# Performance work log

Hardware: AMD Instinct MI355X
Metric: run time of the kernel (lower is better)

Reference implementation:

```python
import jax, jax.numpy as jnp
import numpy as np

C = 512
NUM_HEADS = 8
HEAD_DIM = C // NUM_HEADS


def setup_inputs() -> dict:
    key = jax.random.key(0)
    ks = jax.random.split(key, 9)
    s = 1.0 / np.sqrt(C)
    x = jax.random.normal(ks[0], (8, C, 32, 32), dtype=jnp.float32)
    Wq = jax.random.uniform(ks[1], (C, C), jnp.float32, -s, s)
    bq = jax.random.uniform(ks[2], (C,), jnp.float32, -s, s)
    Wk = jax.random.uniform(ks[3], (C, C), jnp.float32, -s, s)
    bk = jax.random.uniform(ks[4], (C,), jnp.float32, -s, s)
    Wv = jax.random.uniform(ks[5], (C, C), jnp.float32, -s, s)
    bv = jax.random.uniform(ks[6], (C,), jnp.float32, -s, s)
    Wo = jax.random.uniform(ks[7], (C, C), jnp.float32, -s, s)
    bo = jax.random.uniform(ks[8], (C,), jnp.float32, -s, s)
    return {"x": x, "Wq": Wq, "bq": bq, "Wk": Wk, "bk": bk,
            "Wv": Wv, "bv": bv, "Wo": Wo, "bo": bo}


def reference(x, Wq, bq, Wk, bk, Wv, bv, Wo, bo):
    N, Cc, H, W = x.shape
    S = H * W
    # [N, S, C] token sequence
    xs = x.reshape(N, Cc, S).transpose(0, 2, 1)
    # torch Linear: y = x @ W^T + b
    q = xs @ Wq.T + bq
    k = xs @ Wk.T + bk
    v = xs @ Wv.T + bv
    # [N, h, S, d]
    q = q.reshape(N, S, NUM_HEADS, HEAD_DIM).transpose(0, 2, 1, 3)
    k = k.reshape(N, S, NUM_HEADS, HEAD_DIM).transpose(0, 2, 1, 3)
    v = v.reshape(N, S, NUM_HEADS, HEAD_DIM).transpose(0, 2, 1, 3)
    energy = jnp.einsum('nhqd,nhkd->nhqk', q, k)
    attn = jax.nn.softmax(energy / np.sqrt(HEAD_DIM), axis=3)
    out = jnp.einsum('nhql,nhld->nhqd', attn, v)
    # back to [N, S, C]; note torch reshape from (N,h,S,d) order
    out = out.reshape(N, Cc, S) if False else out.reshape(N, -1, Cc)
    out = out @ Wo.T + bo
    return out.reshape(N, Cc, H, W)


if __name__ == "__main__":
    o = reference(**setup_inputs())
    print(o.shape)
```

## Files before the change

### kernel.cpp

```cpp
#include <hip/hip_runtime.h>


typedef _Float16 f16x8 __attribute__((ext_vector_type(8)));
typedef float f32x4 __attribute__((ext_vector_type(4)));

__device__ inline void gl_lds16(const void* g, void* l) {
  __builtin_amdgcn_global_load_lds((const __attribute__((address_space(1))) void*)g,
                                   (__attribute__((address_space(3))) void*)l, 16, 0, 0);
}

__device__ inline float fexp2(float x) {
#if __has_builtin(__builtin_amdgcn_exp2f)
  return __builtin_amdgcn_exp2f(x);
#else
  return exp2f(x);
#endif
}

__global__ void prep_x(const float* __restrict__ x, _Float16* __restrict__ xs16) {
  __shared__ float t[32][33];
  const int n = blockIdx.z;
  const int s0 = blockIdx.x * 32, c0 = blockIdx.y * 32;
  const int tx = threadIdx.x, ty = threadIdx.y;
#pragma unroll
  for (int i = 0; i < 4; ++i) {
    int cc = ty + i * 8;
    t[cc][tx] = x[((size_t)n * 512 + c0 + cc) * 1024 + s0 + tx];
  }
  __syncthreads();
#pragma unroll
  for (int i = 0; i < 4; ++i) {
    int ss = ty + i * 8;
    xs16[((size_t)n * 1024 + s0 + ss) * 512 + c0 + tx] = (_Float16)t[tx][ss];
  }
}

__global__ void prep_w(const float* __restrict__ Wq, const float* __restrict__ bq,
                       const float* __restrict__ Wk, const float* __restrict__ bk,
                       const float* __restrict__ Wv, const float* __restrict__ bv,
                       const float* __restrict__ Wo,
                       _Float16* __restrict__ Wqkv16, float* __restrict__ bqkv,
                       _Float16* __restrict__ Wo16) {
  const float g = 0.18033688011112042f;
  int i = blockIdx.x * 256 + threadIdx.x;
  Wqkv16[i]          = (_Float16)(Wq[i] * g);
  Wqkv16[262144 + i] = (_Float16)Wk[i];
  Wqkv16[524288 + i] = (_Float16)Wv[i];
  Wo16[i]            = (_Float16)Wo[i];
  if (i < 512) {
    bqkv[i]        = bq[i] * g;
    bqkv[512 + i]  = bk[i];
    bqkv[1024 + i] = bv[i];
  }
}

__global__ __launch_bounds__(256, 2) void qkv_gemm(
    const _Float16* __restrict__ A, const _Float16* __restrict__ Bw,
    const float* __restrict__ bias, _Float16* __restrict__ QK,
    _Float16* __restrict__ Vt) {
  __shared__ _Float16 As[128 * 32];
  __shared__ _Float16 Bs[128 * 32];
  const int tid = threadIdx.x;
  const int lane = tid & 63, w = tid >> 6;
  const int quad = lane >> 4, l15 = lane & 15;
  const int bm = blockIdx.x * 128, bn = blockIdx.y * 128;
  const int wr = (w >> 1) * 64, wc = (w & 1) * 64;
  f32x4 acc[4][4] = {};
  for (int k0 = 0; k0 < 512; k0 += 32) {
    __syncthreads();
#pragma unroll
    for (int c = 0; c < 2; ++c) {
      int idx = c * 256 + tid;
      int row = idx >> 2, sc = idx & 3;
      int kg = sc ^ ((row >> 1) & 3);
      gl_lds16(A + (size_t)(bm + row) * 512 + k0 + kg * 8, As + idx * 8);
      gl_lds16(Bw + (size_t)(bn + row) * 512 + k0 + kg * 8, Bs + idx * 8);
    }
    __syncthreads();
    f16x8 af[4], bf[4];
#pragma unroll
    for (int i = 0; i < 4; ++i) {
      int ra = wr + i * 16 + l15;
      af[i] = *(const f16x8*)(As + ra * 32 + (quad ^ ((ra >> 1) & 3)) * 8);
      int rb = wc + i * 16 + l15;
      bf[i] = *(const f16x8*)(Bs + rb * 32 + (quad ^ ((rb >> 1) & 3)) * 8);
    }
#pragma unroll
    for (int i = 0; i < 4; ++i)
#pragma unroll
      for (int j = 0; j < 4; ++j)
        acc[i][j] = __builtin_amdgcn_mfma_f32_16x16x32_f16(af[i], bf[j], acc[i][j], 0, 0, 0);
  }
#pragma unroll
  for (int j = 0; j < 4; ++j) {
    int col = bn + wc + j * 16 + l15;
    float bb = bias[col];
#pragma unroll
    for (int i = 0; i < 4; ++i) {
      int rowb = bm + wr + i * 16 + quad * 4;
#pragma unroll
      for (int r = 0; r < 4; ++r) {
        int m = rowb + r;
        _Float16 hv = (_Float16)(acc[i][j][r] + bb);
        if (col < 1024) {
          QK[(size_t)m * 1024 + col] = hv;
        } else {
          int n = m >> 10, s = m & 1023;
          int hh = (col - 1024) >> 6, d = (col - 1024) & 63;
          int sl = s & 31;
          int p = (s & ~31) | (((sl >> 2) & 3) << 3) | ((sl >> 4) << 2) | (sl & 3);
          Vt[(((size_t)((n * 8 + hh) * 64 + d)) << 10) + p] = hv;
        }
      }
    }
  }
}

__global__ __launch_bounds__(128, 1) void attn(
    const _Float16* __restrict__ QK, const _Float16* __restrict__ Vt,
    _Float16* __restrict__ O16) {
  __shared__ _Float16 Qs[128 * 64];
  __shared__ _Float16 Ks[128 * 64];
  __shared__ _Float16 Vs[64 * 128];
  const int tid = threadIdx.x, lane = tid & 63, w = tid >> 6;
  const int quad = lane >> 4, l15 = lane & 15;
  const int n = blockIdx.y >> 3, h = blockIdx.y & 7;
  const int q0 = blockIdx.x * 128;
#pragma unroll
  for (int c = 0; c < 8; ++c) {
    int idx = c * 128 + tid;
    int row = idx >> 3, sc = idx & 7;
    int dg = sc ^ (row & 7);
    gl_lds16(QK + (size_t)(n * 1024 + q0 + row) * 1024 + h * 64 + dg * 8, Qs + idx * 8);
  }
  __syncthreads();
  f16x8 qf[4][2];
#pragma unroll
  for (int mt = 0; mt < 4; ++mt)
#pragma unroll
    for (int dc = 0; dc < 2; ++dc) {
      int row = w * 64 + mt * 16 + l15;
      qf[mt][dc] = *(const f16x8*)(Qs + row * 64 + ((dc * 4 + quad) ^ (row & 7)) * 8);
    }
  f32x4 oacc[4][4] = {};
  f32x4 lsum[4] = {};
  const f16x8 ones = {(_Float16)1, (_Float16)1, (_Float16)1, (_Float16)1,
                      (_Float16)1, (_Float16)1, (_Float16)1, (_Float16)1};

  for (int kt = 0; kt < 8; ++kt) {
    __syncthreads();
#pragma unroll
    for (int c = 0; c < 8; ++c) {
      int idx = c * 128 + tid;
      int row = idx >> 3, sck = idx & 7;
      int dg = sck ^ (row & 7);
      gl_lds16(QK + (size_t)(n * 1024 + kt * 128 + row) * 1024 + 512 + h * 64 + dg * 8,
               Ks + idx * 8);
      int d = idx >> 4, scv = idx & 15;
      int vg = scv ^ (d & 7);
      gl_lds16(Vt + (size_t)((n * 8 + h) * 64 + d) * 1024 + kt * 128 + vg * 8,
               Vs + idx * 8);
    }
    __syncthreads();
#pragma unroll
    for (int sc = 0; sc < 4; ++sc) {
      f32x4 sacc[4][2] = {};
#pragma unroll
      for (int t = 0; t < 2; ++t) {
        int rk = (sc * 2 + t) * 16 + l15;
        f16x8 kf0 = *(const f16x8*)(Ks + rk * 64 + ((quad) ^ (rk & 7)) * 8);
        f16x8 kf1 = *(const f16x8*)(Ks + rk * 64 + ((4 + quad) ^ (rk & 7)) * 8);
#pragma unroll
        for (int mt = 0; mt < 4; ++mt) {
          sacc[mt][t] = __builtin_amdgcn_mfma_f32_16x16x32_f16(kf0, qf[mt][0], sacc[mt][t], 0, 0, 0);
          sacc[mt][t] = __builtin_amdgcn_mfma_f32_16x16x32_f16(kf1, qf[mt][1], sacc[mt][t], 0, 0, 0);
        }
      }
      f16x8 pf[4];
#pragma unroll
      for (int mt = 0; mt < 4; ++mt) {
#pragma unroll
        for (int t = 0; t < 2; ++t)
#pragma unroll
          for (int r = 0; r < 4; ++r)
            pf[mt][t * 4 + r] = (_Float16)fexp2(sacc[mt][t][r]);
        lsum[mt] = __builtin_amdgcn_mfma_f32_16x16x32_f16(pf[mt], ones, lsum[mt], 0, 0, 0);
      }
#pragma unroll
      for (int nt = 0; nt < 4; ++nt) {
        int rd = nt * 16 + l15;
        f16x8 vf = *(const f16x8*)(Vs + rd * 128 + ((sc * 4 + quad) ^ (rd & 7)) * 8);
#pragma unroll
        for (int mt = 0; mt < 4; ++mt)
          oacc[mt][nt] = __builtin_amdgcn_mfma_f32_16x16x32_f16(pf[mt], vf, oacc[mt][nt], 0, 0, 0);
      }
    }
  }
#pragma unroll
  for (int mt = 0; mt < 4; ++mt) {
#pragma unroll
    for (int r = 0; r < 4; ++r) {
      float rinv = 1.0f / lsum[mt][r];
      int s = q0 + w * 64 + mt * 16 + quad * 4 + r;
      int i = h * 128 + (s >> 3);
      int jb = (s & 7) * 64;
#pragma unroll
      for (int nt = 0; nt < 4; ++nt) {
        int d = nt * 16 + l15;
        O16[(size_t)(n * 1024 + i) * 512 + jb + d] = (_Float16)(oacc[mt][nt][r] * rinv);
      }
    }
  }
}

__global__ __launch_bounds__(256, 2) void out_gemm(
    const _Float16* __restrict__ A, const _Float16* __restrict__ Bw,
    const float* __restrict__ bias, float* __restrict__ out) {
  __shared__ _Float16 As[128 * 32];
  __shared__ _Float16 Bs[128 * 32];
  const int tid = threadIdx.x;
  const int lane = tid & 63, w = tid >> 6;
  const int quad = lane >> 4, l15 = lane & 15;
  const int bm = blockIdx.x * 128, bn = blockIdx.y * 128;
  const int wr = (w >> 1) * 64, wc = (w & 1) * 64;
  f32x4 acc[4][4] = {};
  for (int k0 = 0; k0 < 512; k0 += 32) {
    __syncthreads();
#pragma unroll
    for (int c = 0; c < 2; ++c) {
      int idx = c * 256 + tid;
      int row = idx >> 2, sc = idx & 3;
      int kg = sc ^ ((row >> 1) & 3);
      gl_lds16(A + (size_t)(bm + row) * 512 + k0 + kg * 8, As + idx * 8);
      gl_lds16(Bw + (size_t)(bn + row) * 512 + k0 + kg * 8, Bs + idx * 8);
    }
    __syncthreads();
    f16x8 af[4], bf[4];
#pragma unroll
    for (int i = 0; i < 4; ++i) {
      int ra = wr + i * 16 + l15;
      af[i] = *(const f16x8*)(As + ra * 32 + (quad ^ ((ra >> 1) & 3)) * 8);
      int rb = wc + i * 16 + l15;
      bf[i] = *(const f16x8*)(Bs + rb * 32 + (quad ^ ((rb >> 1) & 3)) * 8);
    }
#pragma unroll
    for (int i = 0; i < 4; ++i)
#pragma unroll
      for (int j = 0; j < 4; ++j)
        acc[i][j] = __builtin_amdgcn_mfma_f32_16x16x32_f16(af[i], bf[j], acc[i][j], 0, 0, 0);
  }
#pragma unroll
  for (int j = 0; j < 4; ++j) {
    int col = bn + wc + j * 16 + l15;
    float bb = bias[col];
#pragma unroll
    for (int i = 0; i < 4; ++i) {
      int rowb = bm + wr + i * 16 + quad * 4;
#pragma unroll
      for (int r = 0; r < 4; ++r)
        out[(size_t)(rowb + r) * 512 + col] = acc[i][j][r] + bb;
    }
  }
}

extern "C" void kernel_launch(void* const* d_in, const int* in_sizes, int n_in,
                              void* d_out, int out_size, void* d_ws, size_t ws_size,
                              hipStream_t stream) {
  const float* x  = (const float*)d_in[0];
  const float* Wq = (const float*)d_in[1];
  const float* bq = (const float*)d_in[2];
  const float* Wk = (const float*)d_in[3];
  const float* bk = (const float*)d_in[4];
  const float* Wv = (const float*)d_in[5];
  const float* bv = (const float*)d_in[6];
  const float* Wo = (const float*)d_in[7];
  const float* bo = (const float*)d_in[8];
  float* out = (float*)d_out;
  char* ws = (char*)d_ws;

  _Float16* xs16   = (_Float16*)(ws);
  _Float16* QK     = (_Float16*)(ws + (8u << 20));
  _Float16* Vt     = (_Float16*)(ws + (24u << 20));
  _Float16* Wqkv16 = (_Float16*)(ws + (32u << 20));
  _Float16* Wo16   = (_Float16*)(ws + (32u << 20) + 1572864);
  float*    bqkv   = (float*)   (ws + (32u << 20) + 2097152);

  hipLaunchKernelGGL(prep_x, dim3(32, 16, 8), dim3(32, 8), 0, stream, x, xs16);
  hipLaunchKernelGGL(prep_w, dim3(1024), dim3(256), 0, stream,
                     Wq, bq, Wk, bk, Wv, bv, Wo, Wqkv16, bqkv, Wo16);
  hipLaunchKernelGGL(qkv_gemm, dim3(64, 12), dim3(256), 0, stream,
                     xs16, Wqkv16, bqkv, QK, Vt);
  hipLaunchKernelGGL(attn, dim3(8, 64), dim3(128), 0, stream, QK, Vt, xs16);
  hipLaunchKernelGGL(out_gemm, dim3(64, 4), dim3(256), 0, stream,
                     xs16, Wo16, bo, out);
}
```

Baseline: 160.7 us.

## Merge prep kernels, coalesce V-transpose stores via LDS, use 4-wave attention blocks

```diff
diff --git a/kernel.cpp b/kernel.cpp
--- a/kernel.cpp
+++ b/kernel.cpp
@@ -2,6 +2,7 @@
 
 
 typedef _Float16 f16x8 __attribute__((ext_vector_type(8)));
+typedef _Float16 f16x4 __attribute__((ext_vector_type(4)));
 typedef float f32x4 __attribute__((ext_vector_type(4)));
 
 __device__ inline void gl_lds16(const void* g, void* l) {
@@ -17,11 +18,32 @@
 #endif
 }
 
-__global__ void prep_x(const float* __restrict__ x, _Float16* __restrict__ xs16) {
+__global__ void prep(const float* __restrict__ x,
+                     const float* __restrict__ Wq, const float* __restrict__ bq,
+                     const float* __restrict__ Wk, const float* __restrict__ bk,
+                     const float* __restrict__ Wv, const float* __restrict__ bv,
+                     const float* __restrict__ Wo,
+                     _Float16* __restrict__ xs16, _Float16* __restrict__ Wqkv16,
+                     float* __restrict__ bqkv, _Float16* __restrict__ Wo16) {
   __shared__ float t[32][33];
-  const int n = blockIdx.z;
-  const int s0 = blockIdx.x * 32, c0 = blockIdx.y * 32;
-  const int tx = threadIdx.x, ty = threadIdx.y;
+  const int tid = threadIdx.x;
+  if (blockIdx.x < 1024) {
+    const float g = 0.18033688011112042f;
+    int i = blockIdx.x * 256 + tid;
+    Wqkv16[i]          = (_Float16)(Wq[i] * g);
+    Wqkv16[262144 + i] = (_Float16)Wk[i];
+    Wqkv16[524288 + i] = (_Float16)Wv[i];
+    Wo16[i]            = (_Float16)Wo[i];
+    if (i < 512) {
+      bqkv[i]        = bq[i] * g;
+      bqkv[512 + i]  = bk[i];
+      bqkv[1024 + i] = bv[i];
+    }
+    return;
+  }
+  const int bid = blockIdx.x - 1024;
+  const int n = bid >> 9, c0 = ((bid >> 5) & 15) * 32, s0 = (bid & 31) * 32;
+  const int tx = tid & 31, ty = tid >> 5;
 #pragma unroll
   for (int i = 0; i < 4; ++i) {
     int cc = ty + i * 8;
@@ -32,25 +54,6 @@
   for (int i = 0; i < 4; ++i) {
     int ss = ty + i * 8;
     xs16[((size_t)n * 1024 + s0 + ss) * 512 + c0 + tx] = (_Float16)t[tx][ss];
-  }
-}
-
-__global__ void prep_w(const float* __restrict__ Wq, const float* __restrict__ bq,
-                       const float* __restrict__ Wk, const float* __restrict__ bk,
-                       const float* __restrict__ Wv, const float* __restrict__ bv,
-                       const float* __restrict__ Wo,
-                       _Float16* __restrict__ Wqkv16, float* __restrict__ bqkv,
-                       _Float16* __restrict__ Wo16) {
-  const float g = 0.18033688011112042f;
-  int i = blockIdx.x * 256 + threadIdx.x;
-  Wqkv16[i]          = (_Float16)(Wq[i] * g);
-  Wqkv16[262144 + i] = (_Float16)Wk[i];
-  Wqkv16[524288 + i] = (_Float16)Wv[i];
-  Wo16[i]            = (_Float16)Wo[i];
-  if (i < 512) {
-    bqkv[i]        = bq[i] * g;
-    bqkv[512 + i]  = bk[i];
-    bqkv[1024 + i] = bv[i];
   }
 }
 
@@ -58,8 +61,9 @@
     const _Float16* __restrict__ A, const _Float16* __restrict__ Bw,
     const float* __restrict__ bias, _Float16* __restrict__ QK,
     _Float16* __restrict__ Vt) {
-  __shared__ _Float16 As[128 * 32];
-  __shared__ _Float16 Bs[128 * 32];
+  __shared__ _Float16 smem[16896];
+  _Float16* As = smem;
+  _Float16* Bs = smem + 4096;
   const int tid = threadIdx.x;
   const int lane = tid & 63, w = tid >> 6;
   const int quad = lane >> 4, l15 = lane & 15;
@@ -91,32 +95,53 @@
       for (int j = 0; j < 4; ++j)
         acc[i][j] = __builtin_amdgcn_mfma_f32_16x16x32_f16(af[i], bf[j], acc[i][j], 0, 0, 0);
   }
-#pragma unroll
-  for (int j = 0; j < 4; ++j) {
-    int col = bn + wc + j * 16 + l15;
-    float bb = bias[col];
-#pragma unroll
-    for (int i = 0; i < 4; ++i) {
-      int rowb = bm + wr + i * 16 + quad * 4;
-#pragma unroll
-      for (int r = 0; r < 4; ++r) {
-        int m = rowb + r;
-        _Float16 hv = (_Float16)(acc[i][j][r] + bb);
-        if (col < 1024) {
-          QK[(size_t)m * 1024 + col] = hv;
-        } else {
-          int n = m >> 10, s = m & 1023;
-          int hh = (col - 1024) >> 6, d = (col - 1024) & 63;
-          int sl = s & 31;
-          int p = (s & ~31) | (((sl >> 2) & 3) << 3) | ((sl >> 4) << 2) | (sl & 3);
-          Vt[(((size_t)((n * 8 + hh) * 64 + d)) << 10) + p] = hv;
-        }
-      }
-    }
-  }
-}
-
-__global__ __launch_bounds__(128, 1) void attn(
+  if (blockIdx.y < 8) {
+#pragma unroll
+    for (int j = 0; j < 4; ++j) {
+      int col = bn + wc + j * 16 + l15;
+      float bb = bias[col];
+#pragma unroll
+      for (int i = 0; i < 4; ++i) {
+        int rowb = bm + wr + i * 16 + quad * 4;
+#pragma unroll
+        for (int r = 0; r < 4; ++r)
+          QK[(size_t)(rowb + r) * 1024 + col] = (_Float16)(acc[i][j][r] + bb);
+      }
+    }
+  } else {
+    __syncthreads();
+#pragma unroll
+    for (int j = 0; j < 4; ++j) {
+      int cl = wc + j * 16 + l15;
+      float bb = bias[bn + cl];
+#pragma unroll
+      for (int i = 0; i < 4; ++i) {
+        int row = wr + i * 16 + quad * 4;
+        f16x4 pk;
+#pragma unroll
+        for (int r = 0; r < 4; ++r) pk[r] = (_Float16)(acc[i][j][r] + bb);
+        *(f16x4*)(smem + cl * 132 + row) = pk;
+      }
+    }
+    __syncthreads();
+    const int n = bm >> 10, s0g = bm & 1023;
+    const int vh = (bn - 1024) >> 6;
+    const int cl = tid >> 1, par = tid & 1;
+    const int hh = vh + (cl >> 6), d = cl & 63;
+    const size_t vrow = (((size_t)((n * 8 + hh) * 64 + d)) << 10) + s0g;
+#pragma unroll
+    for (int g = 0; g < 8; ++g) {
+      int pb = g * 16 + par * 8;
+      int a32 = pb & ~31, q = (pb >> 3) & 3;
+      f16x4 lo = *(const f16x4*)(smem + cl * 132 + a32 + 4 * q);
+      f16x4 hi = *(const f16x4*)(smem + cl * 132 + a32 + 16 + 4 * q);
+      f16x8 o = {lo[0], lo[1], lo[2], lo[3], hi[0], hi[1], hi[2], hi[3]};
+      *(f16x8*)(Vt + vrow + pb) = o;
+    }
+  }
+}
+
+__global__ __launch_bounds__(256, 2) void attn(
     const _Float16* __restrict__ QK, const _Float16* __restrict__ Vt,
     _Float16* __restrict__ O16) {
   __shared__ _Float16 Qs[128 * 64];
@@ -127,31 +152,31 @@
   const int n = blockIdx.y >> 3, h = blockIdx.y & 7;
   const int q0 = blockIdx.x * 128;
 #pragma unroll
-  for (int c = 0; c < 8; ++c) {
-    int idx = c * 128 + tid;
+  for (int c = 0; c < 4; ++c) {
+    int idx = c * 256 + tid;
     int row = idx >> 3, sc = idx & 7;
     int dg = sc ^ (row & 7);
     gl_lds16(QK + (size_t)(n * 1024 + q0 + row) * 1024 + h * 64 + dg * 8, Qs + idx * 8);
   }
   __syncthreads();
-  f16x8 qf[4][2];
-#pragma unroll
-  for (int mt = 0; mt < 4; ++mt)
+  f16x8 qf[2][2];
+#pragma unroll
+  for (int mt = 0; mt < 2; ++mt)
 #pragma unroll
     for (int dc = 0; dc < 2; ++dc) {
-      int row = w * 64 + mt * 16 + l15;
+      int row = w * 32 + mt * 16 + l15;
       qf[mt][dc] = *(const f16x8*)(Qs + row * 64 + ((dc * 4 + quad) ^ (row & 7)) * 8);
     }
-  f32x4 oacc[4][4] = {};
-  f32x4 lsum[4] = {};
+  f32x4 oacc[2][4] = {};
+  f32x4 lsum[2] = {};
   const f16x8 ones = {(_Float16)1, (_Float16)1, (_Float16)1, (_Float16)1,
                       (_Float16)1, (_Float16)1, (_Float16)1, (_Float16)1};
 
   for (int kt = 0; kt < 8; ++kt) {
     __syncthreads();
 #pragma unroll
-    for (int c = 0; c < 8; ++c) {
-      int idx = c * 128 + tid;
+    for (int c = 0; c < 4; ++c) {
+      int idx = c * 256 + tid;
       int row = idx >> 3, sck = idx & 7;
       int dg = sck ^ (row & 7);
       gl_lds16(QK + (size_t)(n * 1024 + kt * 128 + row) * 1024 + 512 + h * 64 + dg * 8,
@@ -164,21 +189,21 @@
     __syncthreads();
 #pragma unroll
     for (int sc = 0; sc < 4; ++sc) {
-      f32x4 sacc[4][2] = {};
+      f32x4 sacc[2][2] = {};
 #pragma unroll
       for (int t = 0; t < 2; ++t) {
         int rk = (sc * 2 + t) * 16 + l15;
         f16x8 kf0 = *(const f16x8*)(Ks + rk * 64 + ((quad) ^ (rk & 7)) * 8);
         f16x8 kf1 = *(const f16x8*)(Ks + rk * 64 + ((4 + quad) ^ (rk & 7)) * 8);
 #pragma unroll
-        for (int mt = 0; mt < 4; ++mt) {
+        for (int mt = 0; mt < 2; ++mt) {
           sacc[mt][t] = __builtin_amdgcn_mfma_f32_16x16x32_f16(kf0, qf[mt][0], sacc[mt][t], 0, 0, 0);
           sacc[mt][t] = __builtin_amdgcn_mfma_f32_16x16x32_f16(kf1, qf[mt][1], sacc[mt][t], 0, 0, 0);
         }
       }
-      f16x8 pf[4];
-#pragma unroll
-      for (int mt = 0; mt < 4; ++mt) {
+      f16x8 pf[2];
+#pragma unroll
+      for (int mt = 0; mt < 2; ++mt) {
 #pragma unroll
         for (int t = 0; t < 2; ++t)
 #pragma unroll
@@ -191,17 +216,17 @@
         int rd = nt * 16 + l15;
         f16x8 vf = *(const f16x8*)(Vs + rd * 128 + ((sc * 4 + quad) ^ (rd & 7)) * 8);
 #pragma unroll
-        for (int mt = 0; mt < 4; ++mt)
+        for (int mt = 0; mt < 2; ++mt)
           oacc[mt][nt] = __builtin_amdgcn_mfma_f32_16x16x32_f16(pf[mt], vf, oacc[mt][nt], 0, 0, 0);
       }
     }
   }
 #pragma unroll
-  for (int mt = 0; mt < 4; ++mt) {
+  for (int mt = 0; mt < 2; ++mt) {
 #pragma unroll
     for (int r = 0; r < 4; ++r) {
       float rinv = 1.0f / lsum[mt][r];
-      int s = q0 + w * 64 + mt * 16 + quad * 4 + r;
+      int s = q0 + w * 32 + mt * 16 + quad * 4 + r;
       int i = h * 128 + (s >> 3);
       int jb = (s & 7) * 64;
 #pragma unroll
@@ -285,12 +310,11 @@
   _Float16* Wo16   = (_Float16*)(ws + (32u << 20) + 1572864);
   float*    bqkv   = (float*)   (ws + (32u << 20) + 2097152);
 
-  hipLaunchKernelGGL(prep_x, dim3(32, 16, 8), dim3(32, 8), 0, stream, x, xs16);
-  hipLaunchKernelGGL(prep_w, dim3(1024), dim3(256), 0, stream,
-                     Wq, bq, Wk, bk, Wv, bv, Wo, Wqkv16, bqkv, Wo16);
+  hipLaunchKernelGGL(prep, dim3(5120), dim3(256), 0, stream,
+                     x, Wq, bq, Wk, bk, Wv, bv, Wo, xs16, Wqkv16, bqkv, Wo16);
   hipLaunchKernelGGL(qkv_gemm, dim3(64, 12), dim3(256), 0, stream,
                      xs16, Wqkv16, bqkv, QK, Vt);
-  hipLaunchKernelGGL(attn, dim3(8, 64), dim3(128), 0, stream, QK, Vt, xs16);
+  hipLaunchKernelGGL(attn, dim3(8, 64), dim3(256), 0, stream, QK, Vt, xs16);
   hipLaunchKernelGGL(out_gemm, dim3(64, 4), dim3(256), 0, stream,
                      xs16, Wo16, bo, out);
 }
```

Result: faster. 144.6 us (-10.0%).
